# Kernel optimization log

Measured on AMD Instinct MI355X. Metric: run time of the kernel, lower is better.

## Reference

```python
import jax, jax.numpy as jnp
import numpy as np

N_NODES = 50000


def _add_self_loops(edge_index, n):
    loop = jnp.arange(n, dtype=edge_index.dtype)
    src = jnp.concatenate([edge_index[0], loop])
    dst = jnp.concatenate([edge_index[1], loop])
    return src, dst


def _gcn_norm(src, dst, n):
    # symmetric normalization with unit edge weights (edge_weight=None)
    w = jnp.ones(src.shape[0], dtype=jnp.float32)
    deg = jax.ops.segment_sum(w, dst, num_segments=n)  # [N]
    dinv = jnp.where(deg > 0, jax.lax.rsqrt(jnp.maximum(deg, 1.0)), 0.0)
    return dinv[src] * w * dinv[dst]  # [E+N]


def _gcn_conv(x, src, dst, norm, W, b, n):
    h = x @ W                                   # [N, out] transform first (PyG order)
    msg = h[src] * norm[:, None]                # [E+N, out] gather + scale
    agg = jax.ops.segment_sum(msg, dst, num_segments=n)  # scatter-add
    return agg + b


def setup_inputs() -> dict:
    key = jax.random.key(0)
    k1, k2, k3, k4 = jax.random.split(key, 4)
    N, E, IN, HID, OUT = N_NODES, 1600000, 512, 64, 7
    x = jax.random.normal(k1, (N, IN), dtype=jnp.float32)
    edge_index = jax.random.randint(k2, (2, E), 0, N, dtype=jnp.int64)
    W1 = jax.random.normal(k3, (IN, HID), dtype=jnp.float32) * (1.0 / np.sqrt(IN))
    b1 = jnp.zeros((HID,), dtype=jnp.float32)
    W2 = jax.random.normal(k4, (HID, OUT), dtype=jnp.float32) * (1.0 / np.sqrt(HID))
    b2 = jnp.zeros((OUT,), dtype=jnp.float32)
    return {"x": x, "edge_index": edge_index, "W1": W1, "b1": b1, "W2": W2, "b2": b2}


def reference(x, edge_index, W1, b1, W2, b2):
    n = x.shape[0]
    src, dst = _add_self_loops(edge_index, n)
    norm = _gcn_norm(src, dst, n)  # graph-only, shared across layers
    h = _gcn_conv(x, src, dst, norm, W1, b1, n)
    h = jax.nn.relu(h)
    # dropout is identity in eval/inference mode
    out = _gcn_conv(h, src, dst, norm, W2, b2, n)
    return out
```

## Files before the change

kernel.cpp:

```cpp
#include <hip/hip_runtime.h>

#define N_NODES 50000
#define N_EDGES 1600000
#define DIM_IN  512
#define DIM_HID 64
#define DIM_OUT 7
#define NBUCK   196
#define PART_BLOCKS 256
#define BCAP    16384

using u16 = unsigned short;
using bf16x8 = __attribute__((ext_vector_type(8))) __bf16;
using f32x4  = __attribute__((ext_vector_type(4))) float;

__device__ __forceinline__ float bf2f(u16 u) {
    union { float f; unsigned int i; } v;
    v.i = ((unsigned int)u) << 16;
    return v.f;
}

__device__ __forceinline__ u16 f2bf(float f) {
    union { float f; unsigned int i; } v;
    v.f = f;
    unsigned int r = 0x7FFFu + ((v.i >> 16) & 1u);
    return (u16)((v.i + r) >> 16);
}

__device__ __forceinline__ float bflo(unsigned int u) {
    union { float f; unsigned int i; } v;
    v.i = u << 16;
    return v.f;
}

__device__ __forceinline__ float bfhi(unsigned int u) {
    union { float f; unsigned int i; } v;
    v.i = u & 0xFFFF0000u;
    return v.f;
}

__device__ __forceinline__ int ld_edge(const int* ei, int i64f, size_t idx) {
    if (i64f) return ei[2 * idx];
    return ei[idx];
}

__launch_bounds__(1024)
__global__ void k_tw1(const u16* __restrict__ xw, const int* __restrict__ ei32,
                      const void* __restrict__ W1, int* __restrict__ flags,
                      int* __restrict__ gcnt, u16* __restrict__ W1T) {
    __shared__ int s1[256];
    __shared__ int s2[256];
    __shared__ int f32s;
    int t = threadIdx.x;
    if (t < 256) {
        u16 w = xw[2 * t];
        int e = (w >> 7) & 0xFF;
        s1[t] = (e >= 100 && e <= 140) ? 1 : 0;
        s2[t] = (ei32[2 * t + 1] != 0) ? 1 : 0;
    }
    __syncthreads();
    for (int off = 128; off >= 1; off >>= 1) {
        if (t < off) { s1[t] += s1[t + off]; s2[t] += s2[t + off]; }
        __syncthreads();
    }
    if (t == 0) f32s = (s1[0] >= 200) ? 0 : 1;
    if (blockIdx.x == 0) {
        if (t == 0) {
            flags[0] = (s1[0] >= 200) ? 0 : 1;
            flags[1] = (s2[0] == 0) ? 1 : 0;
        }
        if (t < NBUCK) gcnt[t] = 0;
    }
    __syncthreads();
    int f32f = f32s;
    int i = blockIdx.x * 1024 + t;
    if (i < DIM_IN * DIM_HID) {
        int n = i >> 9;
        int k = i & 511;
        if (f32f) W1T[i] = f2bf(((const float*)W1)[k * DIM_HID + n]);
        else      W1T[i] = ((const u16*)W1)[k * DIM_HID + n];
    }
}

__launch_bounds__(1024)
__global__ void k_scat(const int* __restrict__ ei, const int* __restrict__ flags,
                       int* __restrict__ gcnt, unsigned int* __restrict__ ebuf) {
    __shared__ int hist[NBUCK];
    __shared__ int cur[NBUCK];
    int t = threadIdx.x, blk = blockIdx.x;
    int i64f = flags[1];
    const int CH = (N_EDGES + PART_BLOCKS - 1) / PART_BLOCKS;
    int lo = blk * CH;
    int hi = lo + CH; if (hi > N_EDGES) hi = N_EDGES;
    if (t < NBUCK) hist[t] = 0;
    __syncthreads();
    for (int i = lo + t; i < hi; i += 1024) {
        int s = ld_edge(ei, i64f, (size_t)i);
        int d = ld_edge(ei, i64f, (size_t)N_EDGES + i);
        if ((unsigned)d < (unsigned)N_NODES && (unsigned)s < (unsigned)N_NODES)
            atomicAdd(&hist[d >> 8], 1);
    }
    __syncthreads();
    if (t < NBUCK) {
        int h = hist[t];
        cur[t] = (h > 0) ? atomicAdd(&gcnt[t], h) : 0;
    }
    __syncthreads();
    for (int i = lo + t; i < hi; i += 1024) {
        int s = ld_edge(ei, i64f, (size_t)i);
        int d = ld_edge(ei, i64f, (size_t)N_EDGES + i);
        if ((unsigned)d < (unsigned)N_NODES && (unsigned)s < (unsigned)N_NODES) {
            int b = d >> 8;
            int off = atomicAdd(&cur[b], 1);
            if ((unsigned)off < (unsigned)BCAP)
                ebuf[(size_t)b * BCAP + off] = ((unsigned)s << 8) | (unsigned)(d & 255);
        }
    }
}

__launch_bounds__(1024)
__global__ void k_cfill(const unsigned int* __restrict__ ebuf,
                        const int* __restrict__ gcnt,
                        int* __restrict__ rowptr, float* __restrict__ dinv,
                        int* __restrict__ col) {
    __shared__ int gs[256];
    __shared__ int dcnt[256];
    __shared__ int sc[256];
    __shared__ int cur[256];
    int b = blockIdx.x, t = threadIdx.x;
    if (t < 256) {
        int gv = (t < NBUCK) ? gcnt[t] : 0;
        if (gv > BCAP) gv = BCAP;
        gs[t] = gv;
    }
    __syncthreads();
    for (int off = 1; off < 256; off <<= 1) {
        int u = (t >= off && t < 256) ? gs[t - off] : 0;
        __syncthreads();
        if (t < 256) gs[t] += u;
        __syncthreads();
    }
    int cntb = gcnt[b]; if (cntb > BCAP) cntb = BCAP;
    int cb = gs[b] - cntb;
    if (b == 0 && t == 0) rowptr[N_NODES] = gs[255];
    const unsigned int* eb = ebuf + (size_t)b * BCAP;

    if (t < 256) dcnt[t] = 0;
    __syncthreads();
    for (int e = t; e < cntb; e += 1024)
        atomicAdd(&dcnt[eb[e] & 255u], 1);
    __syncthreads();
    int v = 0;
    if (t < 256) { v = dcnt[t]; sc[t] = v; }
    __syncthreads();
    for (int off = 1; off < 256; off <<= 1) {
        int u = (t >= off && t < 256) ? sc[t - off] : 0;
        __syncthreads();
        if (t < 256) sc[t] += u;
        __syncthreads();
    }
    if (t < 256) {
        int row0 = cb + sc[t] - v;
        cur[t] = row0;
        int idx = b * 256 + t;
        if (idx < N_NODES) {
            rowptr[idx] = row0;
            dinv[idx] = rsqrtf((float)(v + 1));
        }
    }
    __syncthreads();
    for (int e = t; e < cntb; e += 1024) {
        unsigned int x = eb[e];
        int p = atomicAdd(&cur[x & 255u], 1);
        if ((unsigned)p < (unsigned)N_EDGES) col[p] = (int)(x >> 8);
    }
}

__launch_bounds__(256)
__global__ void k_gemm1(const void* __restrict__ xraw, const u16* __restrict__ W1T,
                        const int* __restrict__ flags, const float* __restrict__ dinv,
                        u16* __restrict__ hs) {
    int f32f = flags[0];
    int wave = threadIdx.x >> 6;
    int lane = threadIdx.x & 63;
    int m16 = lane & 15;
    int quad = lane >> 4;
    int rbase = blockIdx.x * 64 + wave * 16;
    int ra = rbase + m16;
    if (ra > N_NODES - 1) ra = N_NODES - 1;
    const u16*   xrow_b = (const u16*)xraw   + (size_t)ra * DIM_IN + quad * 8;
    const float* xrow_f = (const float*)xraw + (size_t)ra * DIM_IN + quad * 8;
    const u16* wrow = W1T + (size_t)m16 * DIM_IN + quad * 8;

    f32x4 acc0 = {0.f, 0.f, 0.f, 0.f};
    f32x4 acc1 = {0.f, 0.f, 0.f, 0.f};
    f32x4 acc2 = {0.f, 0.f, 0.f, 0.f};
    f32x4 acc3 = {0.f, 0.f, 0.f, 0.f};

    for (int ks = 0; ks < DIM_IN / 32; ++ks) {
        bf16x8 a;
        if (f32f) {
            const float4* q = reinterpret_cast<const float4*>(xrow_f + ks * 32);
            float4 p0 = q[0], p1 = q[1];
            union { bf16x8 v; u16 s[8]; } u;
            u.s[0] = f2bf(p0.x); u.s[1] = f2bf(p0.y); u.s[2] = f2bf(p0.z); u.s[3] = f2bf(p0.w);
            u.s[4] = f2bf(p1.x); u.s[5] = f2bf(p1.y); u.s[6] = f2bf(p1.z); u.s[7] = f2bf(p1.w);
            a = u.v;
        } else {
            a = *reinterpret_cast<const bf16x8*>(xrow_b + ks * 32);
        }
        bf16x8 b0 = *reinterpret_cast<const bf16x8*>(wrow + ks * 32);
        bf16x8 b1 = *reinterpret_cast<const bf16x8*>(wrow + ks * 32 + 16 * DIM_IN);
        bf16x8 b2 = *reinterpret_cast<const bf16x8*>(wrow + ks * 32 + 32 * DIM_IN);
        bf16x8 b3 = *reinterpret_cast<const bf16x8*>(wrow + ks * 32 + 48 * DIM_IN);
        acc0 = __builtin_amdgcn_mfma_f32_16x16x32_bf16(a, b0, acc0, 0, 0, 0);
        acc1 = __builtin_amdgcn_mfma_f32_16x16x32_bf16(a, b1, acc1, 0, 0, 0);
        acc2 = __builtin_amdgcn_mfma_f32_16x16x32_bf16(a, b2, acc2, 0, 0, 0);
        acc3 = __builtin_amdgcn_mfma_f32_16x16x32_bf16(a, b3, acc3, 0, 0, 0);
    }

#pragma unroll
    for (int i = 0; i < 4; ++i) {
        int r = rbase + quad * 4 + i;
        if (r < N_NODES) {
            float dv = dinv[r];
            u16* orow = hs + (size_t)r * DIM_HID;
            orow[ 0 + m16] = f2bf(acc0[i] * dv);
            orow[16 + m16] = f2bf(acc1[i] * dv);
            orow[32 + m16] = f2bf(acc2[i] * dv);
            orow[48 + m16] = f2bf(acc3[i] * dv);
        }
    }
}

__launch_bounds__(256)
__global__ void k_agg1(const u16* __restrict__ hs, const int* __restrict__ rowptr,
                       const int* __restrict__ col, const float* __restrict__ dinv,
                       const void* __restrict__ b1, const void* __restrict__ W2,
                       const int* __restrict__ flags, float* __restrict__ zs) {
    __shared__ float xh[4][64];
    int f32f = flags[0];
    int wave = threadIdx.x >> 6;
    int lane = threadIdx.x & 63;
    int g = lane >> 3;
    int q = lane & 7;
    int d = blockIdx.x * 4 + wave;
    int start = rowptr[d], end = rowptr[d + 1];
    if (start < 0) start = 0;
    if (end > N_EDGES) end = N_EDGES;
    if (end < start) end = start;

    float a[8];
#pragma unroll
    for (int k = 0; k < 8; ++k) a[k] = 0.f;

    const uint4* hs4 = reinterpret_cast<const uint4*>(hs);
    const int* cp = col + start;
    int ne = end - start;
    int nfull = ne >> 3;

    int it = 0;
    for (; it + 4 <= nfull; it += 4) {
        int c0 = cp[(it + 0) * 8 + g];
        int c1 = cp[(it + 1) * 8 + g];
        int c2 = cp[(it + 2) * 8 + g];
        int c3 = cp[(it + 3) * 8 + g];
        uint4 r0 = hs4[(size_t)c0 * 8 + q];
        uint4 r1 = hs4[(size_t)c1 * 8 + q];
        uint4 r2 = hs4[(size_t)c2 * 8 + q];
        uint4 r3 = hs4[(size_t)c3 * 8 + q];
#pragma unroll
        for (int u = 0; u < 4; ++u) {
            uint4 r = (u == 0) ? r0 : (u == 1) ? r1 : (u == 2) ? r2 : r3;
            a[0] += bflo(r.x); a[1] += bfhi(r.x);
            a[2] += bflo(r.y); a[3] += bfhi(r.y);
            a[4] += bflo(r.z); a[5] += bfhi(r.z);
            a[6] += bflo(r.w); a[7] += bfhi(r.w);
        }
    }
    for (; it < nfull; ++it) {
        int c = cp[it * 8 + g];
        uint4 r = hs4[(size_t)c * 8 + q];
        a[0] += bflo(r.x); a[1] += bfhi(r.x);
        a[2] += bflo(r.y); a[3] += bfhi(r.y);
        a[4] += bflo(r.z); a[5] += bfhi(r.z);
        a[6] += bflo(r.w); a[7] += bfhi(r.w);
    }
    {
        int e = start + nfull * 8 + g;
        if (e < end) {
            int c = col[e];
            uint4 r = hs4[(size_t)c * 8 + q];
            a[0] += bflo(r.x); a[1] += bfhi(r.x);
            a[2] += bflo(r.y); a[3] += bfhi(r.y);
            a[4] += bflo(r.z); a[5] += bfhi(r.z);
            a[6] += bflo(r.w); a[7] += bfhi(r.w);
        }
    }

#pragma unroll
    for (int k = 0; k < 8; ++k) {
        a[k] += __shfl_xor(a[k], 8);
        a[k] += __shfl_xor(a[k], 16);
        a[k] += __shfl_xor(a[k], 32);
    }

    {
        uint4 r = hs4[(size_t)d * 8 + q];
        a[0] += bflo(r.x); a[1] += bfhi(r.x);
        a[2] += bflo(r.y); a[3] += bfhi(r.y);
        a[4] += bflo(r.z); a[5] += bfhi(r.z);
        a[6] += bflo(r.w); a[7] += bfhi(r.w);
    }

    float dv = dinv[d];
    float h[8];
    if (f32f) {
        const float* bf = (const float*)b1 + q * 8;
#pragma unroll
        for (int k = 0; k < 8; ++k) h[k] = fmaxf(a[k] * dv + bf[k], 0.f);
    } else {
        const u16* bb = (const u16*)b1 + q * 8;
#pragma unroll
        for (int k = 0; k < 8; ++k) h[k] = fmaxf(a[k] * dv + bf2f(bb[k]), 0.f);
    }

    if (g == 0) {
#pragma unroll
        for (int k = 0; k < 8; ++k) xh[wave][q * 8 + k] = h[k];
    }
    __syncthreads();
    float h2 = xh[wave][lane];

    float p[7];
#pragma unroll
    for (int f = 0; f < 7; ++f) {
        float w = f32f ? ((const float*)W2)[lane * DIM_OUT + f]
                       : bf2f(((const u16*)W2)[lane * DIM_OUT + f]);
        p[f] = h2 * w;
    }
#pragma unroll
    for (int off = 32; off >= 1; off >>= 1) {
#pragma unroll
        for (int f = 0; f < 7; ++f) p[f] += __shfl_xor(p[f], off);
    }
    if (lane == 0) {
#pragma unroll
        for (int f = 0; f < 7; ++f) zs[(size_t)d * 8 + f] = p[f] * dv;
        zs[(size_t)d * 8 + 7] = 0.f;
    }
}

__launch_bounds__(256)
__global__ void k_agg2(const float* __restrict__ zs, const int* __restrict__ rowptr,
                       const int* __restrict__ col, const float* __restrict__ dinv,
                       const void* __restrict__ b2, const int* __restrict__ flags,
                       float* __restrict__ out) {
    int f32f = flags[0];
    int wave = threadIdx.x >> 6;
    int lane = threadIdx.x & 63;
    int d = blockIdx.x * 4 + wave;
    if (d >= N_NODES) return;
    int f = lane & 7;
    int g = lane >> 3;
    int start = rowptr[d], end = rowptr[d + 1];
    if (start < 0) start = 0;
    if (end > N_EDGES) end = N_EDGES;
    if (end < start) end = start;

    float acc = 0.f;
    for (int base = start; base < end; base += 64) {
        int rem = end - base; if (rem > 64) rem = 64;
        int ce = base + lane;
        int c = (ce < end) ? col[ce] : 0;
        float vv[8];
#pragma unroll
        for (int j = 0; j < 8; ++j) {
            int cj = __shfl(c, j * 8 + g);
            vv[j] = (j * 8 + g < rem) ? zs[(size_t)cj * 8 + f] : 0.f;
        }
#pragma unroll
        for (int j = 0; j < 8; ++j) acc += vv[j];
    }

    acc += __shfl_xor(acc, 8);
    acc += __shfl_xor(acc, 16);
    acc += __shfl_xor(acc, 32);

    if (lane < 7) {
        float b2v = f32f ? ((const float*)b2)[lane] : bf2f(((const u16*)b2)[lane]);
        float tot = (acc + zs[(size_t)d * 8 + lane]) * dinv[d] + b2v;
        out[(size_t)d * DIM_OUT + lane] = tot;
    }
}

extern "C" void kernel_launch(void* const* d_in, const int* in_sizes, int n_in,
                              void* d_out, int out_size, void* d_ws, size_t ws_size,
                              hipStream_t stream) {
    const void* x  = d_in[0];
    const int*  ei = (const int*)d_in[1];
    const void* W1 = d_in[2];
    const void* b1 = d_in[3];
    const void* W2 = d_in[4];
    const void* b2 = d_in[5];

    char* ws = (char*)d_ws;
    size_t off = 0;
    auto alloc = [&](size_t bytes) -> void* {
        void* p = ws + off;
        off = (off + bytes + 255) & ~(size_t)255;
        return p;
    };
    int*   flags  = (int*)alloc(32);
    int*   rowptr = (int*)alloc((size_t)(N_NODES + 1) * 4);
    int*   gcnt   = (int*)alloc((size_t)NBUCK * 4);
    float* dinv   = (float*)alloc((size_t)N_NODES * 4);
    u16*   W1T    = (u16*)alloc((size_t)DIM_IN * DIM_HID * 2);
    unsigned int* ebuf = (unsigned int*)alloc((size_t)NBUCK * BCAP * 4);
    int*   colb   = (int*)alloc((size_t)N_EDGES * 4);
    u16*   hs     = (u16*)alloc((size_t)N_NODES * DIM_HID * 2);
    float* zs     = (float*)alloc((size_t)N_NODES * 8 * 4);
    float* out    = (float*)d_out;

    k_tw1   <<<32, 1024, 0, stream>>>((const u16*)x, ei, W1, flags, gcnt, W1T);
    k_scat  <<<PART_BLOCKS, 1024, 0, stream>>>(ei, flags, gcnt, ebuf);
    k_cfill <<<NBUCK, 1024, 0, stream>>>(ebuf, gcnt, rowptr, dinv, colb);
    k_gemm1 <<<(N_NODES + 63) / 64, 256, 0, stream>>>(x, W1T, flags, dinv, hs);
    k_agg1  <<<(N_NODES + 3) / 4, 256, 0, stream>>>(hs, rowptr, colb, dinv, b1, W2, flags, zs);
    k_agg2  <<<(N_NODES + 3) / 4, 256, 0, stream>>>(zs, rowptr, colb, dinv, b2, flags, out);
}
```

Measured before the change: 283.1 us.

## Split hidden features into two column halves and aggregate each in separate passes

The GEMM output is stored as two separate 32-column bf16 planes instead of one 64-column array, and the first-layer aggregation runs twice, once per half. Each gather now touches a 3.2 MB plane, which is meant to stay in cache better and spread edge loads across more lanes (16 edges per wave step). The first half stores a partial second-layer projection in a new buffer and the second half finishes it. The cost is reading the CSR col array twice, an extra kernel launch, and extra partial-sum traffic.

```diff
diff --git a/kernel.cpp b/kernel.cpp
--- a/kernel.cpp
+++ b/kernel.cpp
@@ -223,26 +223,28 @@
         int r = rbase + quad * 4 + i;
         if (r < N_NODES) {
             float dv = dinv[r];
-            u16* orow = hs + (size_t)r * DIM_HID;
-            orow[ 0 + m16] = f2bf(acc0[i] * dv);
-            orow[16 + m16] = f2bf(acc1[i] * dv);
-            orow[32 + m16] = f2bf(acc2[i] * dv);
-            orow[48 + m16] = f2bf(acc3[i] * dv);
+            u16* orowA = hs + (size_t)r * 32;
+            u16* orowB = hs + (size_t)N_NODES * 32 + (size_t)r * 32;
+            orowA[ 0 + m16] = f2bf(acc0[i] * dv);
+            orowA[16 + m16] = f2bf(acc1[i] * dv);
+            orowB[ 0 + m16] = f2bf(acc2[i] * dv);
+            orowB[16 + m16] = f2bf(acc3[i] * dv);
         }
     }
 }
 
 __launch_bounds__(256)
-__global__ void k_agg1(const u16* __restrict__ hs, const int* __restrict__ rowptr,
-                       const int* __restrict__ col, const float* __restrict__ dinv,
-                       const void* __restrict__ b1, const void* __restrict__ W2,
-                       const int* __restrict__ flags, float* __restrict__ zs) {
-    __shared__ float xh[4][64];
+__global__ void k_agg1h(const u16* __restrict__ hsh, const int* __restrict__ rowptr,
+                        const int* __restrict__ col, const float* __restrict__ dinv,
+                        const void* __restrict__ b1, const void* __restrict__ W2,
+                        const int* __restrict__ flags, int half,
+                        float* __restrict__ pacc, float* __restrict__ zs) {
+    __shared__ float xh[4][32];
     int f32f = flags[0];
     int wave = threadIdx.x >> 6;
     int lane = threadIdx.x & 63;
-    int g = lane >> 3;
-    int q = lane & 7;
+    int g = lane >> 2;
+    int q = lane & 3;
     int d = blockIdx.x * 4 + wave;
     int start = rowptr[d], end = rowptr[d + 1];
     if (start < 0) start = 0;
@@ -253,21 +255,21 @@
 #pragma unroll
     for (int k = 0; k < 8; ++k) a[k] = 0.f;
 
-    const uint4* hs4 = reinterpret_cast<const uint4*>(hs);
+    const uint4* h4 = reinterpret_cast<const uint4*>(hsh);
     const int* cp = col + start;
     int ne = end - start;
-    int nfull = ne >> 3;
+    int nfull = ne >> 4;
 
     int it = 0;
     for (; it + 4 <= nfull; it += 4) {
-        int c0 = cp[(it + 0) * 8 + g];
-        int c1 = cp[(it + 1) * 8 + g];
-        int c2 = cp[(it + 2) * 8 + g];
-        int c3 = cp[(it + 3) * 8 + g];
-        uint4 r0 = hs4[(size_t)c0 * 8 + q];
-        uint4 r1 = hs4[(size_t)c1 * 8 + q];
-        uint4 r2 = hs4[(size_t)c2 * 8 + q];
-        uint4 r3 = hs4[(size_t)c3 * 8 + q];
+        int c0 = cp[(it + 0) * 16 + g];
+        int c1 = cp[(it + 1) * 16 + g];
+        int c2 = cp[(it + 2) * 16 + g];
+        int c3 = cp[(it + 3) * 16 + g];
+        uint4 r0 = h4[(size_t)c0 * 4 + q];
+        uint4 r1 = h4[(size_t)c1 * 4 + q];
+        uint4 r2 = h4[(size_t)c2 * 4 + q];
+        uint4 r3 = h4[(size_t)c3 * 4 + q];
 #pragma unroll
         for (int u = 0; u < 4; ++u) {
             uint4 r = (u == 0) ? r0 : (u == 1) ? r1 : (u == 2) ? r2 : r3;
@@ -278,18 +280,18 @@
         }
     }
     for (; it < nfull; ++it) {
-        int c = cp[it * 8 + g];
-        uint4 r = hs4[(size_t)c * 8 + q];
+        int c = cp[it * 16 + g];
+        uint4 r = h4[(size_t)c * 4 + q];
         a[0] += bflo(r.x); a[1] += bfhi(r.x);
         a[2] += bflo(r.y); a[3] += bfhi(r.y);
         a[4] += bflo(r.z); a[5] += bfhi(r.z);
         a[6] += bflo(r.w); a[7] += bfhi(r.w);
     }
     {
-        int e = start + nfull * 8 + g;
+        int e = start + nfull * 16 + g;
         if (e < end) {
             int c = col[e];
-            uint4 r = hs4[(size_t)c * 8 + q];
+            uint4 r = h4[(size_t)c * 4 + q];
             a[0] += bflo(r.x); a[1] += bfhi(r.x);
             a[2] += bflo(r.y); a[3] += bfhi(r.y);
             a[4] += bflo(r.z); a[5] += bfhi(r.z);
@@ -299,13 +301,14 @@
 
 #pragma unroll
     for (int k = 0; k < 8; ++k) {
+        a[k] += __shfl_xor(a[k], 4);
         a[k] += __shfl_xor(a[k], 8);
         a[k] += __shfl_xor(a[k], 16);
         a[k] += __shfl_xor(a[k], 32);
     }
 
     {
-        uint4 r = hs4[(size_t)d * 8 + q];
+        uint4 r = h4[(size_t)d * 4 + q];
         a[0] += bflo(r.x); a[1] += bfhi(r.x);
         a[2] += bflo(r.y); a[3] += bfhi(r.y);
         a[4] += bflo(r.z); a[5] += bfhi(r.z);
@@ -314,12 +317,13 @@
 
     float dv = dinv[d];
     float h[8];
+    int cbase = half * 32 + q * 8;
     if (f32f) {
-        const float* bf = (const float*)b1 + q * 8;
+        const float* bf = (const float*)b1 + cbase;
 #pragma unroll
         for (int k = 0; k < 8; ++k) h[k] = fmaxf(a[k] * dv + bf[k], 0.f);
     } else {
-        const u16* bb = (const u16*)b1 + q * 8;
+        const u16* bb = (const u16*)b1 + cbase;
 #pragma unroll
         for (int k = 0; k < 8; ++k) h[k] = fmaxf(a[k] * dv + bf2f(bb[k]), 0.f);
     }
@@ -329,13 +333,14 @@
         for (int k = 0; k < 8; ++k) xh[wave][q * 8 + k] = h[k];
     }
     __syncthreads();
-    float h2 = xh[wave][lane];
+    float h2 = (lane < 32) ? xh[wave][lane] : 0.f;
+    int wr = half * 32 + (lane & 31);
 
     float p[7];
 #pragma unroll
     for (int f = 0; f < 7; ++f) {
-        float w = f32f ? ((const float*)W2)[lane * DIM_OUT + f]
-                       : bf2f(((const u16*)W2)[lane * DIM_OUT + f]);
+        float w = f32f ? ((const float*)W2)[wr * DIM_OUT + f]
+                       : bf2f(((const u16*)W2)[wr * DIM_OUT + f]);
         p[f] = h2 * w;
     }
 #pragma unroll
@@ -344,9 +349,15 @@
         for (int f = 0; f < 7; ++f) p[f] += __shfl_xor(p[f], off);
     }
     if (lane == 0) {
-#pragma unroll
-        for (int f = 0; f < 7; ++f) zs[(size_t)d * 8 + f] = p[f] * dv;
-        zs[(size_t)d * 8 + 7] = 0.f;
+        if (half == 0) {
+#pragma unroll
+            for (int f = 0; f < 7; ++f) pacc[(size_t)d * 8 + f] = p[f];
+        } else {
+#pragma unroll
+            for (int f = 0; f < 7; ++f)
+                zs[(size_t)d * 8 + f] = (p[f] + pacc[(size_t)d * 8 + f]) * dv;
+            zs[(size_t)d * 8 + 7] = 0.f;
+        }
     }
 }
 
@@ -418,13 +429,17 @@
     unsigned int* ebuf = (unsigned int*)alloc((size_t)NBUCK * BCAP * 4);
     int*   colb   = (int*)alloc((size_t)N_EDGES * 4);
     u16*   hs     = (u16*)alloc((size_t)N_NODES * DIM_HID * 2);
+    float* pacc   = (float*)alloc((size_t)N_NODES * 8 * 4);
     float* zs     = (float*)alloc((size_t)N_NODES * 8 * 4);
     float* out    = (float*)d_out;
+
+    u16* hsB = hs + (size_t)N_NODES * 32;
 
     k_tw1   <<<32, 1024, 0, stream>>>((const u16*)x, ei, W1, flags, gcnt, W1T);
     k_scat  <<<PART_BLOCKS, 1024, 0, stream>>>(ei, flags, gcnt, ebuf);
     k_cfill <<<NBUCK, 1024, 0, stream>>>(ebuf, gcnt, rowptr, dinv, colb);
     k_gemm1 <<<(N_NODES + 63) / 64, 256, 0, stream>>>(x, W1T, flags, dinv, hs);
-    k_agg1  <<<(N_NODES + 3) / 4, 256, 0, stream>>>(hs, rowptr, colb, dinv, b1, W2, flags, zs);
+    k_agg1h <<<(N_NODES + 3) / 4, 256, 0, stream>>>(hs,  rowptr, colb, dinv, b1, W2, flags, 0, pacc, zs);
+    k_agg1h <<<(N_NODES + 3) / 4, 256, 0, stream>>>(hsB, rowptr, colb, dinv, b1, W2, flags, 1, pacc, zs);
     k_agg2  <<<(N_NODES + 3) / 4, 256, 0, stream>>>(zs, rowptr, colb, dinv, b2, flags, out);
 }
```

Measured after the change: 326.4 us. 1.15x slower.
